# Optimization experiments

Measured on AMD Instinct MI355X. Metric: run time of the kernel, lower is better.

Reference implementation:

```python
import jax, jax.numpy as jnp
import numpy as np

B, S, H, L, NH, F, V, K, R = 64, 512, 256, 4, 8, 1024, 50265, 8, 25
DH = H // NH
EPS = 1e-5


def layernorm(x, g, b):
    mu = x.mean(-1, keepdims=True)
    var = ((x - mu) ** 2).mean(-1, keepdims=True)
    return (x - mu) * jax.lax.rsqrt(var + EPS) * g + b


def setup_inputs() -> dict:
    key = jax.random.key(0)
    ks = jax.random.split(key, 24)
    input_ids = jax.random.randint(ks[0], (B, S), 0, V, dtype=jnp.int64)
    # prefix attention mask with variable valid lengths (ragged sequences)
    lengths = jax.random.randint(ks[1], (B,), 16, S + 1)
    attention_mask = (jnp.arange(S)[None, :] < lengths[:, None]).astype(jnp.int32)
    sub_indices = jax.random.randint(ks[2], (B, K), 0, S, dtype=jnp.int64)
    obj_indices = jax.random.randint(ks[3], (B, K), 0, S, dtype=jnp.int64)
    sub_counts = jax.random.randint(ks[4], (B,), 0, K + 1, dtype=jnp.int32)
    obj_counts = jax.random.randint(ks[5], (B,), 0, K + 1, dtype=jnp.int32)
    sc = 0.02
    p = {
        'emb': jax.random.normal(ks[6], (V, H), jnp.float32) * sc,
        'Wqkv': jax.random.normal(ks[7], (L, H, 3 * H), jnp.float32) * sc,
        'bqkv': jnp.zeros((L, 3 * H), jnp.float32),
        'Wo': jax.random.normal(ks[8], (L, H, H), jnp.float32) * sc,
        'bo': jnp.zeros((L, H), jnp.float32),
        'ln1_g': jnp.ones((L, H), jnp.float32), 'ln1_b': jnp.zeros((L, H), jnp.float32),
        'ln2_g': jnp.ones((L, H), jnp.float32), 'ln2_b': jnp.zeros((L, H), jnp.float32),
        'W1': jax.random.normal(ks[9], (L, H, F), jnp.float32) * sc,
        'b1': jnp.zeros((L, F), jnp.float32),
        'W2': jax.random.normal(ks[10], (L, F, H), jnp.float32) * sc,
        'b2': jnp.zeros((L, H), jnp.float32),
        'lnf_g': jnp.ones((H,), jnp.float32), 'lnf_b': jnp.zeros((H,), jnp.float32),
        'mW1': jax.random.normal(ks[11], (3 * H, H), jnp.float32) * sc,
        'mb1': jnp.zeros((H,), jnp.float32),
        'mW2': jax.random.normal(ks[12], (H, R), jnp.float32) * sc,
        'mb2': jnp.zeros((R,), jnp.float32),
    }
    return dict(input_ids=input_ids, attention_mask=attention_mask,
                sub_indices=sub_indices, sub_counts=sub_counts,
                obj_indices=obj_indices, obj_counts=obj_counts, **p)


def _encoder(input_ids, attention_mask, emb, Wqkv, bqkv, Wo, bo,
             ln1_g, ln1_b, ln2_g, ln2_b, W1, b1, W2, b2, lnf_g, lnf_b):
    x = emb[input_ids]  # [B,S,H]
    kbias = jnp.where(attention_mask[:, None, None, :] > 0, 0.0, -1e9)  # mask keys
    scale = 1.0 / np.sqrt(DH)
    for l in range(L):  # small fixed layer loop
        qkv = x @ Wqkv[l] + bqkv[l]
        q, k, v = jnp.split(qkv, 3, axis=-1)
        q = q.reshape(B, S, NH, DH).transpose(0, 2, 1, 3)
        k = k.reshape(B, S, NH, DH).transpose(0, 2, 1, 3)
        v = v.reshape(B, S, NH, DH).transpose(0, 2, 1, 3)
        scores = jnp.einsum('bhqd,bhkd->bhqk', q, k) * scale + kbias
        attn = jax.nn.softmax(scores, axis=-1)
        o = jnp.einsum('bhqk,bhkd->bhqd', attn, v).transpose(0, 2, 1, 3).reshape(B, S, H)
        x = layernorm(x + o @ Wo[l] + bo[l], ln1_g[l], ln1_b[l])
        h = jax.nn.relu(x @ W1[l] + b1[l]) @ W2[l] + b2[l]
        x = layernorm(x + h, ln2_g[l], ln2_b[l])
    return layernorm(x, lnf_g, lnf_b)


def _pooled(seq, idx, counts):
    g = jnp.take_along_axis(seq, idx[:, :, None], axis=1)  # [B,K,H]
    m = (jnp.arange(K)[None, :] < counts[:, None]).astype(seq.dtype)
    s = (g * m[:, :, None]).sum(1)
    c = counts.astype(seq.dtype)[:, None]
    return jnp.where(c > 0, s / jnp.maximum(c, 1.0), 0.0)  # zeros if no indices


def reference(input_ids, attention_mask, sub_indices, sub_counts, obj_indices, obj_counts,
              emb, Wqkv, bqkv, Wo, bo, ln1_g, ln1_b, ln2_g, ln2_b,
              W1, b1, W2, b2, lnf_g, lnf_b, mW1, mb1, mW2, mb2):
    seq = _encoder(input_ids, attention_mask, emb, Wqkv, bqkv, Wo, bo,
                   ln1_g, ln1_b, ln2_g, ln2_b, W1, b1, W2, b2, lnf_g, lnf_b)
    sub = _pooled(seq, sub_indices, sub_counts)
    obj = _pooled(seq, obj_indices, obj_counts)
    mask = attention_mask.astype(seq.dtype)
    lens = mask.sum(1)[:, None]
    story = jnp.where(lens > 0, (seq * mask[:, :, None]).sum(1) / jnp.maximum(lens, 1.0),
                      seq.mean(1))
    feat = jnp.concatenate([sub, obj, story], axis=-1)  # [B,3H]
    logits = jax.nn.relu(feat @ mW1 + mb1) @ mW2 + mb2
    return logits
```

## Files before the change

kernel.cpp:

```cpp
#include <hip/hip_runtime.h>
#include <hip/hip_bf16.h>


typedef __hip_bfloat16 bf16;
typedef __attribute__((ext_vector_type(8))) short short8;
typedef __attribute__((ext_vector_type(4))) float f32x4;

#define S_LEN 512
#define H_DIM 256
#define NTOK  32768
#define QSCALE 0.25503488f

__device__ __forceinline__ void gload_lds16(const void* g, void* l) {
  __builtin_amdgcn_global_load_lds(
      (const __attribute__((address_space(1))) unsigned int*)g,
      (__attribute__((address_space(3))) unsigned int*)l, 16, 0, 0);
}

__device__ __forceinline__ unsigned short f2bu(float x) {
  bf16 t = __float2bfloat16(x);
  return *reinterpret_cast<unsigned short*>(&t);
}

__global__ __launch_bounds__(64) void lens_kernel(
    const int* __restrict__ amask, int* __restrict__ ntiles,
    int* __restrict__ lenb) {
  const int b = blockIdx.x, t = threadIdx.x;
  int c = 0;
#pragma unroll
  for (int i = 0; i < 8; ++i) c += amask[b * S_LEN + t + i * 64];
#pragma unroll
  for (int off = 1; off < 64; off <<= 1) c += __shfl_xor(c, off);
  if (t == 0) {
    lenb[b] = c;
    ntiles[b] = (c + 63) >> 6;
  }
}

__global__ __launch_bounds__(64) void order_kernel(
    const int* __restrict__ ntiles, int* __restrict__ ordb) {
  const int b = threadIdx.x;
  const int ntb = ntiles[b];
  int rank = 0;
  for (int j = 0; j < 64; ++j) {
    const int ntj = __shfl(ntb, j);
    rank += (ntj > ntb) || (ntj == ntb && j < b);
  }
  ordb[rank] = b;
}

__global__ __launch_bounds__(256) void tcast_kernel(
    const float* __restrict__ in, bf16* __restrict__ out, int K, int N) {
  const int l = blockIdx.z;
  in  += (size_t)l * K * N;
  out += (size_t)l * K * N;
  __shared__ float t[32][33];
  const int n0 = blockIdx.x * 32, k0 = blockIdx.y * 32;
  const int c = threadIdx.x & 31, r = threadIdx.x >> 5;
#pragma unroll
  for (int rr = r; rr < 32; rr += 8)
    t[rr][c] = in[(size_t)(k0 + rr) * N + n0 + c];
  __syncthreads();
#pragma unroll
  for (int rr = r; rr < 32; rr += 8)
    out[(size_t)(n0 + rr) * K + k0 + c] = __float2bfloat16(t[c][rr]);
}

__global__ __launch_bounds__(256) void embed_kernel(
    const int* __restrict__ ids, const float* __restrict__ emb,
    float* __restrict__ X, bf16* __restrict__ Xb) {
  size_t i4 = (size_t)blockIdx.x * 256 + threadIdx.x;
  int tok = (int)(i4 >> 6);
  int d4  = (int)(i4 & 63);
  float4 v = *(const float4*)&emb[(size_t)ids[tok] * H_DIM + d4 * 4];
  *(float4*)&X[i4 * 4] = v;
  ushort4 pk;
  pk.x = f2bu(v.x); pk.y = f2bu(v.y); pk.z = f2bu(v.z); pk.w = f2bu(v.w);
  *(ushort4*)&Xb[i4 * 4] = pk;
}

#define SRC_CHUNK(tid_) (((tid_) & 3) ^ (((tid_) >> 3) & 3))

template<int MODE, bool RELU>
__global__ __launch_bounds__(256) void hgemm_kernel(
    const bf16* __restrict__ A, const bf16* __restrict__ Bt,
    const float* __restrict__ bias, float* __restrict__ Cf,
    bf16* __restrict__ Cb, bf16* __restrict__ Vt,
    int M, int N, int K) {
  __shared__ __align__(16) bf16 As[2][4096];
  __shared__ __align__(16) bf16 Bs[2][4096];
  const int tid = threadIdx.x;
  const int wv = tid >> 6, ln = tid & 63;
  const int fr = ln & 15, g4 = ln >> 4;
  const int wr = wv >> 1, wc = wv & 1;
  const int m0 = blockIdx.x * 128, n0 = blockIdx.y * 128;
  const int lr = tid >> 2;
  const int lk = SRC_CHUNK(tid) * 8;
  const int rc = (g4 ^ ((fr >> 1) & 3)) * 8;

#define STAGE_G(buf, kk) do {                                                  \
    const int kof_ = (kk) * 32;                                                \
    gload_lds16(A  + (size_t)(m0 + lr) * K + kof_ + lk,                        \
                &As[(buf)][wv * 512]);                                         \
    gload_lds16(A  + (size_t)(m0 + 64 + lr) * K + kof_ + lk,                   \
                &As[(buf)][2048 + wv * 512]);                                  \
    gload_lds16(Bt + (size_t)(n0 + lr) * K + kof_ + lk,                        \
                &Bs[(buf)][wv * 512]);                                         \
    gload_lds16(Bt + (size_t)(n0 + 64 + lr) * K + kof_ + lk,                   \
                &Bs[(buf)][2048 + wv * 512]);                                  \
  } while (0)

  f32x4 acc[4][4];
#pragma unroll
  for (int i = 0; i < 4; ++i)
#pragma unroll
    for (int j = 0; j < 4; ++j)
      acc[i][j] = (f32x4){0.f, 0.f, 0.f, 0.f};

  const int NT = K >> 5;
  STAGE_G(0, 0);
  __syncthreads();
  int cur = 0;
  for (int kt = 0; kt < NT; ++kt) {
    if (kt + 1 < NT) STAGE_G(cur ^ 1, kt + 1);
    short8 af[4], bfv[4];
#pragma unroll
    for (int i = 0; i < 4; ++i)
      af[i] = *(const short8*)&As[cur][(wr * 64 + i * 16 + fr) * 32 + rc];
#pragma unroll
    for (int j = 0; j < 4; ++j)
      bfv[j] = *(const short8*)&Bs[cur][(wc * 64 + j * 16 + fr) * 32 + rc];
#pragma unroll
    for (int i = 0; i < 4; ++i)
#pragma unroll
      for (int j = 0; j < 4; ++j)
        acc[i][j] = __builtin_amdgcn_mfma_f32_16x16x32_bf16(
            af[i], bfv[j], acc[i][j], 0, 0, 0);
    __syncthreads();
    cur ^= 1;
  }
#undef STAGE_G

  const int crow = g4 * 4, ccol = fr;
#pragma unroll
  for (int j = 0; j < 4; ++j) {
    const int n = n0 + wc * 64 + j * 16 + ccol;
    const float bv = bias[n];
#pragma unroll
    for (int i = 0; i < 4; ++i) {
      const int mbase = m0 + wr * 64 + i * 16 + crow;
#pragma unroll
      for (int r = 0; r < 4; ++r) {
        float o = acc[i][j][r] + bv;
        if (RELU) o = fmaxf(o, 0.f);
        const int m = mbase + r;
        if (MODE == 1) {
          Cb[(size_t)m * N + n] = __float2bfloat16(o);
        } else {
          if (n < 512) {
            const float oo = (n < 256) ? o * QSCALE : o;
            Cb[(size_t)m * 768 + n] = __float2bfloat16(oo);
          } else {
            const int hd = n - 512, hh = hd >> 5, dd = hd & 31;
            const int bb = m >> 9, ss = m & 511;
            const int ssw = (ss & ~63) | ((ss & 63) ^ ((dd & 7) << 3));
            Vt[(((size_t)bb * 8 + hh) * 32 + dd) * 512 + ssw] =
                __float2bfloat16(o);
          }
        }
      }
    }
  }
}

__global__ __launch_bounds__(256) void hgemm_ln_kernel(
    const bf16* __restrict__ A, const bf16* __restrict__ Bt,
    const float* __restrict__ bias, float* __restrict__ X,
    bf16* __restrict__ Xb, const float* __restrict__ g,
    const float* __restrict__ bt, int K) {
  __shared__ __align__(16) bf16 As[2][2048];
  __shared__ __align__(16) bf16 Bs[2][8192];
  __shared__ float rsum[4][64];
  __shared__ float rsq[4][64];
  const int tid = threadIdx.x;
  const int wv = tid >> 6;
  const int ln = tid & 63;
  const int fr = ln & 15, g4 = ln >> 4;
  const int m0 = blockIdx.x * 64;
  const int rc = (g4 ^ ((fr >> 1) & 3)) * 8;

#define STAGE_L(buf, kk) do {                                                  \
    const int kof_ = (kk) * 32;                                                \
    gload_lds16(A + (size_t)(m0 + (tid >> 2)) * K + kof_ +                     \
                    SRC_CHUNK(tid) * 8,                                        \
                &As[(buf)][wv * 512]);                                         \
    _Pragma("unroll")                                                          \
    for (int e = 0; e < 4; ++e) {                                              \
      const int vt = e * 256 + tid;                                            \
      gload_lds16(Bt + (size_t)(vt >> 2) * K + kof_ + SRC_CHUNK(vt) * 8,       \
                  &Bs[(buf)][e * 2048 + wv * 512]);                            \
    }                                                                          \
  } while (0)

  f32x4 acc[4][4];
#pragma unroll
  for (int i = 0; i < 4; ++i)
#pragma unroll
    for (int j = 0; j < 4; ++j)
      acc[i][j] = (f32x4){0.f, 0.f, 0.f, 0.f};

  const int NT = K >> 5;
  STAGE_L(0, 0);
  __syncthreads();
  int cur = 0;
  for (int kt = 0; kt < NT; ++kt) {
    if (kt + 1 < NT) STAGE_L(cur ^ 1, kt + 1);
    short8 af[4], bfv[4];
#pragma unroll
    for (int i = 0; i < 4; ++i)
      af[i] = *(const short8*)&As[cur][(i * 16 + fr) * 32 + rc];
#pragma unroll
    for (int j = 0; j < 4; ++j)
      bfv[j] = *(const short8*)&Bs[cur][(wv * 64 + j * 16 + fr) * 32 + rc];
#pragma unroll
    for (int i = 0; i < 4; ++i)
#pragma unroll
      for (int j = 0; j < 4; ++j)
        acc[i][j] = __builtin_amdgcn_mfma_f32_16x16x32_bf16(
            af[i], bfv[j], acc[i][j], 0, 0, 0);
    __syncthreads();
    cur ^= 1;
  }
#undef STAGE_L

  float gj[4], bj[4], bsj[4];
#pragma unroll
  for (int j = 0; j < 4; ++j) {
    const int n = wv * 64 + j * 16 + fr;
    gj[j] = g[n]; bj[j] = bt[n]; bsj[j] = bias[n];
  }
#pragma unroll
  for (int i = 0; i < 4; ++i) {
#pragma unroll
    for (int r = 0; r < 4; ++r) {
      const int m = m0 + i * 16 + g4 * 4 + r;
#pragma unroll
      for (int j = 0; j < 4; ++j)
        acc[i][j][r] += bsj[j] + X[(size_t)m * 256 + wv * 64 + j * 16 + fr];
    }
  }
#pragma unroll
  for (int i = 0; i < 4; ++i) {
#pragma unroll
    for (int r = 0; r < 4; ++r) {
      float sp = acc[i][0][r] + acc[i][1][r] + acc[i][2][r] + acc[i][3][r];
      float qp = acc[i][0][r] * acc[i][0][r] + acc[i][1][r] * acc[i][1][r] +
                 acc[i][2][r] * acc[i][2][r] + acc[i][3][r] * acc[i][3][r];
#pragma unroll
      for (int off = 1; off < 16; off <<= 1) {
        sp += __shfl_xor(sp, off);
        qp += __shfl_xor(qp, off);
      }
      if (fr == 0) {
        const int ri = i * 16 + g4 * 4 + r;
        rsum[wv][ri] = sp;
        rsq[wv][ri] = qp;
      }
    }
  }
  __syncthreads();
#pragma unroll
  for (int i = 0; i < 4; ++i) {
#pragma unroll
    for (int r = 0; r < 4; ++r) {
      const int ri = i * 16 + g4 * 4 + r;
      const float tot = rsum[0][ri] + rsum[1][ri] + rsum[2][ri] + rsum[3][ri];
      const float tq = rsq[0][ri] + rsq[1][ri] + rsq[2][ri] + rsq[3][ri];
      const float mu = tot * (1.0f / 256.0f);
      const float var = tq * (1.0f / 256.0f) - mu * mu;
      const float rstd = rsqrtf(var + 1e-5f);
      const int m = m0 + ri;
#pragma unroll
      for (int j = 0; j < 4; ++j) {
        const float o = (acc[i][j][r] - mu) * rstd * gj[j] + bj[j];
        const size_t idx = (size_t)m * 256 + wv * 64 + j * 16 + fr;
        X[idx] = o;
        Xb[idx] = __float2bfloat16(o);
      }
    }
  }
}

__global__ __launch_bounds__(256) void attn_mfma_kernel(
    const bf16* __restrict__ QKVb, const bf16* __restrict__ Vt,
    const int* __restrict__ amask, const int* __restrict__ ntiles,
    const int* __restrict__ ordb, bf16* __restrict__ Ob) {
  const int b = ordb[blockIdx.z];
  const int h = blockIdx.y, q0 = blockIdx.x * 64;
  const int tid = threadIdx.x;
  const int wv = tid >> 6, ln = tid & 63;
  const int fr = ln & 15, g4 = ln >> 4;
  const int f8 = (fr & 7) << 3;
  const int rc = (g4 ^ ((fr >> 1) & 3)) * 8;
  const int bh32 = (b * 8 + h) * 32;
  __shared__ __align__(16) bf16 Ks[2][2048];
  __shared__ __align__(16) bf16 Vs[2][2048];
  __shared__ __align__(16) bf16 Ps[4096];
  __shared__ __align__(16) float Ms[64];

  const int nt = ntiles[b];

#define STAGE_A(buf, kt_) do {                                                 \
    const int k0_ = (kt_) * 64;                                                \
    gload_lds16(QKVb + (size_t)(b * S_LEN + k0_ + (tid >> 2)) * 768 + 256 +    \
                    h * 32 + SRC_CHUNK(tid) * 8,                               \
                &Ks[(buf)][wv * 512]);                                         \
    gload_lds16(Vt + (size_t)(bh32 + (tid >> 3)) * 512 + k0_ + (tid & 7) * 8,  \
                &Vs[(buf)][wv * 512]);                                         \
    if ((kt_) == nt - 1 && tid < 64)                                           \
      Ms[tid] = (amask[b * S_LEN + k0_ + tid] != 0) ? 0.f : -1e9f;             \
  } while (0)

  gload_lds16(QKVb + (size_t)(b * S_LEN + q0 + (tid >> 2)) * 768 + h * 32 +
                  SRC_CHUNK(tid) * 8,
              &Ps[wv * 512]);
  STAGE_A(0, 0);
  __syncthreads();
  const short8 qb = *(const short8*)&Ps[(wv * 16 + fr) * 32 + rc];
  __syncthreads();

  f32x4 accO[2];
  accO[0] = (f32x4){0.f, 0.f, 0.f, 0.f};
  accO[1] = (f32x4){0.f, 0.f, 0.f, 0.f};
  float mrun = -1e30f, lrun = 0.f;
  const int srcq = 20 * g4;

  int cur = 0;
  for (int kt = 0; kt < nt; ++kt) {
    if (kt + 1 < nt) STAGE_A(cur ^ 1, kt + 1);
    const bool bnd = (kt == nt - 1);

    f32x4 st[4];
#pragma unroll
    for (int kb = 0; kb < 4; ++kb) {
      const short8 kf = *(const short8*)&Ks[cur][(kb * 16 + fr) * 32 + rc];
      f32x4 z = (f32x4){0.f, 0.f, 0.f, 0.f};
      st[kb] = __builtin_amdgcn_mfma_f32_16x16x32_bf16(kf, qb, z, 0, 0, 0);
    }

    float p[16];
    if (bnd) {
#pragma unroll
      for (int kb = 0; kb < 4; ++kb) {
        const f32x4 mv = ((const f32x4*)Ms)[kb * 4 + g4];
#pragma unroll
        for (int rr = 0; rr < 4; ++rr) p[kb * 4 + rr] = st[kb][rr] + mv[rr];
      }
    } else {
#pragma unroll
      for (int kb = 0; kb < 4; ++kb)
#pragma unroll
        for (int rr = 0; rr < 4; ++rr) p[kb * 4 + rr] = st[kb][rr];
    }

    const float a0 = fmaxf(fmaxf(p[0], p[1]), p[2]);
    const float a1 = fmaxf(fmaxf(p[3], p[4]), p[5]);
    const float a2 = fmaxf(fmaxf(p[6], p[7]), p[8]);
    const float a3 = fmaxf(fmaxf(p[9], p[10]), p[11]);
    const float a4 = fmaxf(fmaxf(p[12], p[13]), p[14]);
    float mx = fmaxf(fmaxf(fmaxf(a0, a1), fmaxf(a2, a3)), fmaxf(a4, p[15]));
    mx = fmaxf(mx, __shfl_xor(mx, 16));
    mx = fmaxf(mx, __shfl_xor(mx, 32));

    float corr = 1.f;
    if (!__all(mx <= mrun + 8.f)) {
      const float mnew = fmaxf(mrun, mx);
      corr = exp2f(mrun - mnew);
      mrun = mnew;
#pragma unroll
      for (int rr = 0; rr < 4; ++rr) {
        const float cs = __shfl(corr, srcq + rr);
        accO[0][rr] *= cs;
        accO[1][rr] *= cs;
      }
    }

#pragma unroll
    for (int i = 0; i < 16; ++i) p[i] = exp2f(p[i] - mrun);
    const float b0 = p[0] + p[1], b1 = p[2] + p[3], b2 = p[4] + p[5],
                b3 = p[6] + p[7], b4 = p[8] + p[9], b5 = p[10] + p[11],
                b6 = p[12] + p[13], b7 = p[14] + p[15];
    float ps = ((b0 + b1) + (b2 + b3)) + ((b4 + b5) + (b6 + b7));
    ps += __shfl_xor(ps, 16);
    ps += __shfl_xor(ps, 32);
    lrun = lrun * corr + ps;

#pragma unroll
    for (int kb = 0; kb < 4; ++kb) {
      ushort4 w4;
      w4.x = f2bu(p[kb * 4 + 0]);
      w4.y = f2bu(p[kb * 4 + 1]);
      w4.z = f2bu(p[kb * 4 + 2]);
      w4.w = f2bu(p[kb * 4 + 3]);
      *(ushort4*)&Ps[wv * 1024 + fr * 64 + ((kb * 16 + g4 * 4) ^ f8)] = w4;
    }

#pragma unroll
    for (int kk = 0; kk < 2; ++kk) {
      const short8 pa = *(const short8*)
          &Ps[wv * 1024 + fr * 64 + ((kk * 32 + g4 * 8) ^ f8)];
#pragma unroll
      for (int df = 0; df < 2; ++df) {
        const short8 vb = *(const short8*)
            &Vs[cur][(df * 16 + fr) * 64 + ((kk * 32 + g4 * 8) ^ f8)];
        accO[df] = __builtin_amdgcn_mfma_f32_16x16x32_bf16(
            pa, vb, accO[df], 0, 0, 0);
      }
    }
    __syncthreads();
    cur ^= 1;
  }
#undef STAGE_A

  const float inv = 1.0f / lrun;
#pragma unroll
  for (int rr = 0; rr < 4; ++rr) {
    const float iv = __shfl(inv, srcq + rr);
    const int q = q0 + wv * 16 + g4 * 4 + rr;
    const size_t orow = ((size_t)b * S_LEN + q) * H_DIM + h * 32;
    Ob[orow + fr]      = __float2bfloat16(accO[0][rr] * iv);
    Ob[orow + 16 + fr] = __float2bfloat16(accO[1][rr] * iv);
  }
}

__global__ __launch_bounds__(256) void lnf_pool_kernel(
    float* __restrict__ X, const float* __restrict__ g,
    const float* __restrict__ bt, const int* __restrict__ amask,
    float* __restrict__ Pstory) {
  const int b = blockIdx.x, sg = blockIdx.y;
  const int tid = threadIdx.x, wv = tid >> 6, ln = tid & 63;
  const float4 gg = ((const float4*)g)[ln];
  const float4 bb = ((const float4*)bt)[ln];
  float ax = 0.f, ay = 0.f, az = 0.f, aw = 0.f;
  for (int t = wv; t < 64; t += 4) {
    const size_t tok = (size_t)b * S_LEN + sg * 64 + t;
    float4 v = ((const float4*)X)[tok * 64 + ln];
    float s = v.x + v.y + v.z + v.w;
#pragma unroll
    for (int off = 1; off < 64; off <<= 1) s += __shfl_xor(s, off);
    const float mu = s * (1.0f / 256.0f);
    const float dx = v.x - mu, dy = v.y - mu, dz = v.z - mu, dw = v.w - mu;
    float sq = dx * dx + dy * dy + dz * dz + dw * dw;
#pragma unroll
    for (int off = 1; off < 64; off <<= 1) sq += __shfl_xor(sq, off);
    const float rstd = rsqrtf(sq * (1.0f / 256.0f) + 1e-5f);
    float4 o;
    o.x = dx * rstd * gg.x + bb.x;
    o.y = dy * rstd * gg.y + bb.y;
    o.z = dz * rstd * gg.z + bb.z;
    o.w = dw * rstd * gg.w + bb.w;
    ((float4*)X)[tok * 64 + ln] = o;
    if (amask[tok]) { ax += o.x; ay += o.y; az += o.z; aw += o.w; }
  }
  __shared__ float part[4][256];
  part[wv][ln * 4 + 0] = ax;
  part[wv][ln * 4 + 1] = ay;
  part[wv][ln * 4 + 2] = az;
  part[wv][ln * 4 + 3] = aw;
  __syncthreads();
  const float tot = part[0][tid] + part[1][tid] + part[2][tid] + part[3][tid];
  Pstory[((size_t)b * 8 + sg) * 256 + tid] = tot;
}

__global__ __launch_bounds__(256) void poolcls_kernel(
    const float* __restrict__ X, const float* __restrict__ Pstory,
    const int* __restrict__ lenb,
    const int* __restrict__ sub_idx, const int* __restrict__ sub_cnt,
    const int* __restrict__ obj_idx, const int* __restrict__ obj_cnt,
    const float* __restrict__ mW1, const float* __restrict__ mb1,
    const float* __restrict__ mW2, const float* __restrict__ mb2,
    float* __restrict__ out) {
  const int b = blockIdx.x, t = threadIdx.x;
  __shared__ float fs[768];
  __shared__ float hid[256];
  const float* xb = X + (size_t)b * S_LEN * H_DIM;
  {
    float s = 0.f;
#pragma unroll
    for (int i = 0; i < 8; ++i) s += Pstory[((size_t)b * 8 + i) * 256 + t];
    fs[512 + t] = s / (float)lenb[b];
  }
  {
    const int cc = sub_cnt[b];
    float s2 = 0.f;
    for (int j = 0; j < cc; ++j)
      s2 += xb[(size_t)sub_idx[b * 8 + j] * H_DIM + t];
    fs[t] = (cc > 0) ? s2 / (float)cc : 0.f;
  }
  {
    const int cc = obj_cnt[b];
    float s2 = 0.f;
    for (int j = 0; j < cc; ++j)
      s2 += xb[(size_t)obj_idx[b * 8 + j] * H_DIM + t];
    fs[256 + t] = (cc > 0) ? s2 / (float)cc : 0.f;
  }
  __syncthreads();
  float acc = mb1[t];
  for (int k = 0; k < 768; ++k) acc += fs[k] * mW1[(size_t)k * 256 + t];
  hid[t] = fmaxf(acc, 0.f);
  __syncthreads();
  if (t < 25) {
    float o = mb2[t];
    for (int j = 0; j < 256; ++j) o += hid[j] * mW2[j * 25 + t];
    out[b * 25 + t] = o;
  }
}

extern "C" void kernel_launch(void* const* d_in, const int* in_sizes, int n_in,
                              void* d_out, int out_size, void* d_ws, size_t ws_size,
                              hipStream_t stream) {
  const int*   input_ids = (const int*)d_in[0];
  const int*   amask     = (const int*)d_in[1];
  const int*   sub_idx   = (const int*)d_in[2];
  const int*   sub_cnt   = (const int*)d_in[3];
  const int*   obj_idx   = (const int*)d_in[4];
  const int*   obj_cnt   = (const int*)d_in[5];
  const float* emb  = (const float*)d_in[6];
  const float* Wqkv = (const float*)d_in[7];
  const float* bqkv = (const float*)d_in[8];
  const float* Wo   = (const float*)d_in[9];
  const float* bo   = (const float*)d_in[10];
  const float* ln1g = (const float*)d_in[11];
  const float* ln1b = (const float*)d_in[12];
  const float* ln2g = (const float*)d_in[13];
  const float* ln2b = (const float*)d_in[14];
  const float* W1   = (const float*)d_in[15];
  const float* b1   = (const float*)d_in[16];
  const float* W2   = (const float*)d_in[17];
  const float* b2   = (const float*)d_in[18];
  const float* lnfg = (const float*)d_in[19];
  const float* lnfb = (const float*)d_in[20];
  const float* mW1  = (const float*)d_in[21];
  const float* mb1  = (const float*)d_in[22];
  const float* mW2  = (const float*)d_in[23];
  const float* mb2  = (const float*)d_in[24];
  float* out = (float*)d_out;

  char* w = (char*)d_ws;
  float* X    = (float*)w;                         w += (size_t)NTOK * 256 * 4;
  bf16*  Xb   = (bf16*)w;                          w += (size_t)NTOK * 256 * 2;
  bf16*  QKVb = (bf16*)w;                          w += (size_t)NTOK * 768 * 2;
  bf16*  Vtg  = (bf16*)w;                          w += (size_t)NTOK * 256 * 2;
  bf16*  Ob   = (bf16*)w;                          w += (size_t)NTOK * 256 * 2;
  bf16*  Wqkvt= (bf16*)w;                          w += (size_t)4 * 768 * 256 * 2;
  bf16*  Wot  = (bf16*)w;                          w += (size_t)4 * 256 * 256 * 2;
  bf16*  W1t  = (bf16*)w;                          w += (size_t)4 * 1024 * 256 * 2;
  bf16*  W2t  = (bf16*)w;                          w += (size_t)4 * 256 * 1024 * 2;
  float* Pstory = (float*)w;                       w += (size_t)64 * 8 * 256 * 4;
  int*   ntiles = (int*)w;                         w += 256;
  int*   lenb   = (int*)w;                         w += 256;
  int*   ordb   = (int*)w;                         w += 256;
  bf16*  Hb   = QKVb;

  lens_kernel<<<64, 64, 0, stream>>>(amask, ntiles, lenb);
  order_kernel<<<1, 64, 0, stream>>>(ntiles, ordb);
  tcast_kernel<<<dim3(24, 8, 4), 256, 0, stream>>>(Wqkv, Wqkvt, 256, 768);
  tcast_kernel<<<dim3(8, 8, 4), 256, 0, stream>>>(Wo, Wot, 256, 256);
  tcast_kernel<<<dim3(32, 8, 4), 256, 0, stream>>>(W1, W1t, 256, 1024);
  tcast_kernel<<<dim3(8, 32, 4), 256, 0, stream>>>(W2, W2t, 1024, 256);

  embed_kernel<<<8192, 256, 0, stream>>>(input_ids, emb, X, Xb);

  for (int l = 0; l < 4; ++l) {
    const bf16* Wqkvt_l = Wqkvt + (size_t)l * 768 * 256;
    const bf16* Wot_l   = Wot + (size_t)l * 256 * 256;
    const bf16* W1t_l   = W1t + (size_t)l * 1024 * 256;
    const bf16* W2t_l   = W2t + (size_t)l * 256 * 1024;

    hgemm_kernel<2, false><<<dim3(256, 6), 256, 0, stream>>>(
        Xb, Wqkvt_l, bqkv + (size_t)l * 768, nullptr, QKVb, Vtg, NTOK, 768, 256);
    attn_mfma_kernel<<<dim3(8, 8, 64), 256, 0, stream>>>(
        QKVb, Vtg, amask, ntiles, ordb, Ob);
    hgemm_ln_kernel<<<512, 256, 0, stream>>>(
        Ob, Wot_l, bo + (size_t)l * 256, X, Xb,
        ln1g + l * 256, ln1b + l * 256, 256);
    hgemm_kernel<1, true><<<dim3(256, 8), 256, 0, stream>>>(
        Xb, W1t_l, b1 + (size_t)l * 1024, nullptr, Hb, nullptr, NTOK, 1024, 256);
    hgemm_ln_kernel<<<512, 256, 0, stream>>>(
        Hb, W2t_l, b2 + (size_t)l * 256, X, Xb,
        ln2g + l * 256, ln2b + l * 256, 1024);
  }
  lnf_pool_kernel<<<dim3(64, 8), 256, 0, stream>>>(X, lnfg, lnfb, amask, Pstory);
  poolcls_kernel<<<64, 256, 0, stream>>>(X, Pstory, lenb, sub_idx, sub_cnt,
                                         obj_idx, obj_cnt, mW1, mb1, mW2, mb2,
                                         out);
}
```

Baseline: 791.1 us.

## Fuse FFN up-projection, ReLU, down-projection and LayerNorm into one kernel

Replaces the separate W1 GEMM and the W2 GEMM+LayerNorm kernels with a single kernel per 64-row tile. The kernel walks the 1024-wide hidden dimension in 256-column chunks, keeps each ReLU'd hidden chunk in LDS as bf16, and accumulates the W2 product in registers before applying residual, bias and LayerNorm. This removes the round trip of the large intermediate activation through global memory. In exchange, each block uses much more LDS and there are fewer blocks, so occupancy and latency hiding drop.

Measured after the change: 828.7 us. 1.05x slower.

```diff
diff --git a/kernel.cpp b/kernel.cpp
--- a/kernel.cpp
+++ b/kernel.cpp
@@ -283,6 +283,185 @@
 #pragma unroll
       for (int j = 0; j < 4; ++j) {
         const float o = (acc[i][j][r] - mu) * rstd * gj[j] + bj[j];
+        const size_t idx = (size_t)m * 256 + wv * 64 + j * 16 + fr;
+        X[idx] = o;
+        Xb[idx] = __float2bfloat16(o);
+      }
+    }
+  }
+}
+
+__global__ __launch_bounds__(256) void ffn_fused_kernel(
+    const bf16* __restrict__ Xbin, const bf16* __restrict__ W1t,
+    const float* __restrict__ b1, const bf16* __restrict__ W2t,
+    const float* __restrict__ b2, float* __restrict__ X,
+    bf16* __restrict__ Xb, const float* __restrict__ g,
+    const float* __restrict__ bt) {
+  __shared__ __align__(16) bf16 As[2][2048];
+  __shared__ __align__(16) bf16 Bs[2][8192];
+  __shared__ __align__(16) bf16 Hs[16384];
+  __shared__ float rsum[4][64];
+  __shared__ float rsq[4][64];
+  const int tid = threadIdx.x;
+  const int wv = tid >> 6, ln = tid & 63;
+  const int fr = ln & 15, g4 = ln >> 4;
+  const int m0 = blockIdx.x * 64;
+  const int rc = (g4 ^ ((fr >> 1) & 3)) * 8;
+
+#define STAGE_FA(buf, kk) do {                                                 \
+    const int kof_ = (kk) * 32;                                                \
+    gload_lds16(Xbin + (size_t)(m0 + (tid >> 2)) * 256 + kof_ +                \
+                    SRC_CHUNK(tid) * 8,                                        \
+                &As[(buf)][wv * 512]);                                         \
+    _Pragma("unroll")                                                          \
+    for (int e = 0; e < 4; ++e) {                                              \
+      const int vt = e * 256 + tid;                                            \
+      gload_lds16(W1t + (size_t)(f0 + (vt >> 2)) * 256 + kof_ +                \
+                      SRC_CHUNK(vt) * 8,                                       \
+                  &Bs[(buf)][e * 2048 + wv * 512]);                            \
+    }                                                                          \
+  } while (0)
+
+#define STAGE_FB(buf, kk) do {                                                 \
+    const int kof_ = f0 + (kk) * 32;                                           \
+    _Pragma("unroll")                                                          \
+    for (int e = 0; e < 4; ++e) {                                              \
+      const int vt = e * 256 + tid;                                            \
+      gload_lds16(W2t + (size_t)(vt >> 2) * 1024 + kof_ + SRC_CHUNK(vt) * 8,   \
+                  &Bs[(buf)][e * 2048 + wv * 512]);                            \
+    }                                                                          \
+  } while (0)
+
+  f32x4 accY[4][4];
+#pragma unroll
+  for (int i = 0; i < 4; ++i)
+#pragma unroll
+    for (int j = 0; j < 4; ++j)
+      accY[i][j] = (f32x4){0.f, 0.f, 0.f, 0.f};
+
+  for (int ch = 0; ch < 4; ++ch) {
+    const int f0 = ch * 256;
+    f32x4 accH[4][4];
+#pragma unroll
+    for (int i = 0; i < 4; ++i)
+#pragma unroll
+      for (int j = 0; j < 4; ++j)
+        accH[i][j] = (f32x4){0.f, 0.f, 0.f, 0.f};
+    STAGE_FA(0, 0);
+    __syncthreads();
+    int cur = 0;
+    for (int kt = 0; kt < 8; ++kt) {
+      if (kt + 1 < 8) STAGE_FA(cur ^ 1, kt + 1);
+      short8 af[4], bfv[4];
+#pragma unroll
+      for (int i = 0; i < 4; ++i)
+        af[i] = *(const short8*)&As[cur][(i * 16 + fr) * 32 + rc];
+#pragma unroll
+      for (int j = 0; j < 4; ++j)
+        bfv[j] = *(const short8*)&Bs[cur][(wv * 64 + j * 16 + fr) * 32 + rc];
+#pragma unroll
+      for (int i = 0; i < 4; ++i)
+#pragma unroll
+        for (int j = 0; j < 4; ++j)
+          accH[i][j] = __builtin_amdgcn_mfma_f32_16x16x32_bf16(
+              af[i], bfv[j], accH[i][j], 0, 0, 0);
+      __syncthreads();
+      cur ^= 1;
+    }
+    float bs1[4];
+#pragma unroll
+    for (int j = 0; j < 4; ++j) bs1[j] = b1[f0 + wv * 64 + j * 16 + fr];
+#pragma unroll
+    for (int i = 0; i < 4; ++i)
+#pragma unroll
+      for (int r = 0; r < 4; ++r) {
+        const int ml = i * 16 + g4 * 4 + r;
+#pragma unroll
+        for (int j = 0; j < 4; ++j) {
+          const int c = wv * 64 + j * 16 + fr;
+          const float h = fmaxf(accH[i][j][r] + bs1[j], 0.f);
+          const int ccp = (c >> 3) ^ (ml & 7);
+          Hs[ml * 256 + ccp * 8 + (c & 7)] = __float2bfloat16(h);
+        }
+      }
+    __syncthreads();
+    STAGE_FB(0, 0);
+    __syncthreads();
+    cur = 0;
+    for (int kt = 0; kt < 8; ++kt) {
+      if (kt + 1 < 8) STAGE_FB(cur ^ 1, kt + 1);
+      short8 af[4], bfv[4];
+#pragma unroll
+      for (int i = 0; i < 4; ++i) {
+        const int ccp = (kt * 4 + g4) ^ (fr & 7);
+        af[i] = *(const short8*)&Hs[(i * 16 + fr) * 256 + ccp * 8];
+      }
+#pragma unroll
+      for (int j = 0; j < 4; ++j)
+        bfv[j] = *(const short8*)&Bs[cur][(wv * 64 + j * 16 + fr) * 32 + rc];
+#pragma unroll
+      for (int i = 0; i < 4; ++i)
+#pragma unroll
+        for (int j = 0; j < 4; ++j)
+          accY[i][j] = __builtin_amdgcn_mfma_f32_16x16x32_bf16(
+              af[i], bfv[j], accY[i][j], 0, 0, 0);
+      __syncthreads();
+      cur ^= 1;
+    }
+  }
+#undef STAGE_FA
+#undef STAGE_FB
+
+  float gj[4], bj[4], bsj[4];
+#pragma unroll
+  for (int j = 0; j < 4; ++j) {
+    const int n = wv * 64 + j * 16 + fr;
+    gj[j] = g[n]; bj[j] = bt[n]; bsj[j] = b2[n];
+  }
+#pragma unroll
+  for (int i = 0; i < 4; ++i) {
+#pragma unroll
+    for (int r = 0; r < 4; ++r) {
+      const int m = m0 + i * 16 + g4 * 4 + r;
+#pragma unroll
+      for (int j = 0; j < 4; ++j)
+        accY[i][j][r] += bsj[j] + X[(size_t)m * 256 + wv * 64 + j * 16 + fr];
+    }
+  }
+#pragma unroll
+  for (int i = 0; i < 4; ++i) {
+#pragma unroll
+    for (int r = 0; r < 4; ++r) {
+      float sp = accY[i][0][r] + accY[i][1][r] + accY[i][2][r] + accY[i][3][r];
+      float qp = accY[i][0][r] * accY[i][0][r] + accY[i][1][r] * accY[i][1][r] +
+                 accY[i][2][r] * accY[i][2][r] + accY[i][3][r] * accY[i][3][r];
+#pragma unroll
+      for (int off = 1; off < 16; off <<= 1) {
+        sp += __shfl_xor(sp, off);
+        qp += __shfl_xor(qp, off);
+      }
+      if (fr == 0) {
+        const int ri = i * 16 + g4 * 4 + r;
+        rsum[wv][ri] = sp;
+        rsq[wv][ri] = qp;
+      }
+    }
+  }
+  __syncthreads();
+#pragma unroll
+  for (int i = 0; i < 4; ++i) {
+#pragma unroll
+    for (int r = 0; r < 4; ++r) {
+      const int ri = i * 16 + g4 * 4 + r;
+      const float tot = rsum[0][ri] + rsum[1][ri] + rsum[2][ri] + rsum[3][ri];
+      const float tq = rsq[0][ri] + rsq[1][ri] + rsq[2][ri] + rsq[3][ri];
+      const float mu = tot * (1.0f / 256.0f);
+      const float var = tq * (1.0f / 256.0f) - mu * mu;
+      const float rstd = rsqrtf(var + 1e-5f);
+      const int m = m0 + ri;
+#pragma unroll
+      for (int j = 0; j < 4; ++j) {
+        const float o = (accY[i][j][r] - mu) * rstd * gj[j] + bj[j];
         const size_t idx = (size_t)m * 256 + wv * 64 + j * 16 + fr;
         X[idx] = o;
         Xb[idx] = __float2bfloat16(o);
@@ -560,7 +739,6 @@
   int*   ntiles = (int*)w;                         w += 256;
   int*   lenb   = (int*)w;                         w += 256;
   int*   ordb   = (int*)w;                         w += 256;
-  bf16*  Hb   = QKVb;
 
   lens_kernel<<<64, 64, 0, stream>>>(amask, ntiles, lenb);
   order_kernel<<<1, 64, 0, stream>>>(ntiles, ordb);
@@ -584,11 +762,9 @@
     hgemm_ln_kernel<<<512, 256, 0, stream>>>(
         Ob, Wot_l, bo + (size_t)l * 256, X, Xb,
         ln1g + l * 256, ln1b + l * 256, 256);
-    hgemm_kernel<1, true><<<dim3(256, 8), 256, 0, stream>>>(
-        Xb, W1t_l, b1 + (size_t)l * 1024, nullptr, Hb, nullptr, NTOK, 1024, 256);
-    hgemm_ln_kernel<<<512, 256, 0, stream>>>(
-        Hb, W2t_l, b2 + (size_t)l * 256, X, Xb,
-        ln2g + l * 256, ln2b + l * 256, 1024);
+    ffn_fused_kernel<<<512, 256, 0, stream>>>(
+        Xb, W1t_l, b1 + (size_t)l * 1024, W2t_l, b2 + (size_t)l * 256,
+        X, Xb, ln2g + l * 256, ln2b + l * 256);
   }
   lnf_pool_kernel<<<dim3(64, 8), 256, 0, stream>>>(X, lnfg, lnfb, amask, Pstory);
   poolcls_kernel<<<64, 256, 0, stream>>>(X, Pstory, lenb, sub_idx, sub_cnt,
```

## Process four query tiles per attention block to reuse staged K/V tiles

Applied to the files above, without the earlier changes.

Each attention workgroup now handles 256 query rows, four 64-row sub-tiles, instead of 64. Every K/V tile staged into LDS is therefore reused for four query tiles, cutting global loads of K/V and the number of staging and barrier steps. In exchange the grid shrinks fourfold to 1024 blocks, and per-thread register use rises with four sets of accumulators, running max and running sum, which may lower occupancy. All four sub-tiles also share one key-tile count, so query sub-tiles still run the full key loop.

Measured after the change: 825.1 us. 1.04x slower.

```diff
diff --git a/kernel.cpp b/kernel.cpp
--- a/kernel.cpp
+++ b/kernel.cpp
@@ -296,7 +296,8 @@
     const int* __restrict__ amask, const int* __restrict__ ntiles,
     const int* __restrict__ ordb, bf16* __restrict__ Ob) {
   const int b = ordb[blockIdx.z];
-  const int h = blockIdx.y, q0 = blockIdx.x * 64;
+  const int h = blockIdx.y;
+  const int q_base = blockIdx.x * 256;
   const int tid = threadIdx.x;
   const int wv = tid >> 6, ln = tid & 63;
   const int fr = ln & 15, g4 = ln >> 4;
@@ -321,18 +322,31 @@
       Ms[tid] = (amask[b * S_LEN + k0_ + tid] != 0) ? 0.f : -1e9f;             \
   } while (0)
 
-  gload_lds16(QKVb + (size_t)(b * S_LEN + q0 + (tid >> 2)) * 768 + h * 32 +
-                  SRC_CHUNK(tid) * 8,
-              &Ps[wv * 512]);
   STAGE_A(0, 0);
-  __syncthreads();
-  const short8 qb = *(const short8*)&Ps[(wv * 16 + fr) * 32 + rc];
-  __syncthreads();
-
-  f32x4 accO[2];
-  accO[0] = (f32x4){0.f, 0.f, 0.f, 0.f};
-  accO[1] = (f32x4){0.f, 0.f, 0.f, 0.f};
-  float mrun = -1e30f, lrun = 0.f;
+
+  short8 qb[4];
+#pragma unroll
+  for (int t2 = 0; t2 < 2; ++t2) {
+    gload_lds16(QKVb + (size_t)(b * S_LEN + q_base + t2 * 128 + (tid >> 2)) *
+                        768 + h * 32 + SRC_CHUNK(tid) * 8,
+                &Ps[wv * 512]);
+    gload_lds16(QKVb + (size_t)(b * S_LEN + q_base + t2 * 128 + 64 +
+                                (tid >> 2)) * 768 + h * 32 + SRC_CHUNK(tid) * 8,
+                &Ps[2048 + wv * 512]);
+    __syncthreads();
+    qb[t2 * 2]     = *(const short8*)&Ps[(wv * 16 + fr) * 32 + rc];
+    qb[t2 * 2 + 1] = *(const short8*)&Ps[2048 + (wv * 16 + fr) * 32 + rc];
+    __syncthreads();
+  }
+
+  f32x4 accO[4][2];
+#pragma unroll
+  for (int t = 0; t < 4; ++t) {
+    accO[t][0] = (f32x4){0.f, 0.f, 0.f, 0.f};
+    accO[t][1] = (f32x4){0.f, 0.f, 0.f, 0.f};
+  }
+  float mrun[4] = {-1e30f, -1e30f, -1e30f, -1e30f};
+  float lrun[4] = {0.f, 0.f, 0.f, 0.f};
   const int srcq = 20 * g4;
 
   int cur = 0;
@@ -340,81 +354,85 @@
     if (kt + 1 < nt) STAGE_A(cur ^ 1, kt + 1);
     const bool bnd = (kt == nt - 1);
 
-    f32x4 st[4];
-#pragma unroll
-    for (int kb = 0; kb < 4; ++kb) {
-      const short8 kf = *(const short8*)&Ks[cur][(kb * 16 + fr) * 32 + rc];
-      f32x4 z = (f32x4){0.f, 0.f, 0.f, 0.f};
-      st[kb] = __builtin_amdgcn_mfma_f32_16x16x32_bf16(kf, qb, z, 0, 0, 0);
-    }
-
-    float p[16];
-    if (bnd) {
+#pragma unroll
+    for (int t = 0; t < 4; ++t) {
+      f32x4 st[4];
 #pragma unroll
       for (int kb = 0; kb < 4; ++kb) {
-        const f32x4 mv = ((const f32x4*)Ms)[kb * 4 + g4];
-#pragma unroll
-        for (int rr = 0; rr < 4; ++rr) p[kb * 4 + rr] = st[kb][rr] + mv[rr];
-      }
-    } else {
-#pragma unroll
-      for (int kb = 0; kb < 4; ++kb)
-#pragma unroll
-        for (int rr = 0; rr < 4; ++rr) p[kb * 4 + rr] = st[kb][rr];
-    }
-
-    const float a0 = fmaxf(fmaxf(p[0], p[1]), p[2]);
-    const float a1 = fmaxf(fmaxf(p[3], p[4]), p[5]);
-    const float a2 = fmaxf(fmaxf(p[6], p[7]), p[8]);
-    const float a3 = fmaxf(fmaxf(p[9], p[10]), p[11]);
-    const float a4 = fmaxf(fmaxf(p[12], p[13]), p[14]);
-    float mx = fmaxf(fmaxf(fmaxf(a0, a1), fmaxf(a2, a3)), fmaxf(a4, p[15]));
-    mx = fmaxf(mx, __shfl_xor(mx, 16));
-    mx = fmaxf(mx, __shfl_xor(mx, 32));
-
-    float corr = 1.f;
-    if (!__all(mx <= mrun + 8.f)) {
-      const float mnew = fmaxf(mrun, mx);
-      corr = exp2f(mrun - mnew);
-      mrun = mnew;
-#pragma unroll
-      for (int rr = 0; rr < 4; ++rr) {
-        const float cs = __shfl(corr, srcq + rr);
-        accO[0][rr] *= cs;
-        accO[1][rr] *= cs;
-      }
-    }
-
-#pragma unroll
-    for (int i = 0; i < 16; ++i) p[i] = exp2f(p[i] - mrun);
-    const float b0 = p[0] + p[1], b1 = p[2] + p[3], b2 = p[4] + p[5],
-                b3 = p[6] + p[7], b4 = p[8] + p[9], b5 = p[10] + p[11],
-                b6 = p[12] + p[13], b7 = p[14] + p[15];
-    float ps = ((b0 + b1) + (b2 + b3)) + ((b4 + b5) + (b6 + b7));
-    ps += __shfl_xor(ps, 16);
-    ps += __shfl_xor(ps, 32);
-    lrun = lrun * corr + ps;
-
-#pragma unroll
-    for (int kb = 0; kb < 4; ++kb) {
-      ushort4 w4;
-      w4.x = f2bu(p[kb * 4 + 0]);
-      w4.y = f2bu(p[kb * 4 + 1]);
-      w4.z = f2bu(p[kb * 4 + 2]);
-      w4.w = f2bu(p[kb * 4 + 3]);
-      *(ushort4*)&Ps[wv * 1024 + fr * 64 + ((kb * 16 + g4 * 4) ^ f8)] = w4;
-    }
-
-#pragma unroll
-    for (int kk = 0; kk < 2; ++kk) {
-      const short8 pa = *(const short8*)
-          &Ps[wv * 1024 + fr * 64 + ((kk * 32 + g4 * 8) ^ f8)];
-#pragma unroll
-      for (int df = 0; df < 2; ++df) {
-        const short8 vb = *(const short8*)
-            &Vs[cur][(df * 16 + fr) * 64 + ((kk * 32 + g4 * 8) ^ f8)];
-        accO[df] = __builtin_amdgcn_mfma_f32_16x16x32_bf16(
-            pa, vb, accO[df], 0, 0, 0);
+        const short8 kf =
+            *(const short8*)&Ks[cur][(kb * 16 + fr) * 32 + rc];
+        f32x4 z = (f32x4){0.f, 0.f, 0.f, 0.f};
+        st[kb] = __builtin_amdgcn_mfma_f32_16x16x32_bf16(kf, qb[t], z, 0, 0, 0);
+      }
+
+      float p[16];
+      if (bnd) {
+#pragma unroll
+        for (int kb = 0; kb < 4; ++kb) {
+          const f32x4 mv = ((const f32x4*)Ms)[kb * 4 + g4];
+#pragma unroll
+          for (int rr = 0; rr < 4; ++rr) p[kb * 4 + rr] = st[kb][rr] + mv[rr];
+        }
+      } else {
+#pragma unroll
+        for (int kb = 0; kb < 4; ++kb)
+#pragma unroll
+          for (int rr = 0; rr < 4; ++rr) p[kb * 4 + rr] = st[kb][rr];
+      }
+
+      const float a0 = fmaxf(fmaxf(p[0], p[1]), p[2]);
+      const float a1 = fmaxf(fmaxf(p[3], p[4]), p[5]);
+      const float a2 = fmaxf(fmaxf(p[6], p[7]), p[8]);
+      const float a3 = fmaxf(fmaxf(p[9], p[10]), p[11]);
+      const float a4 = fmaxf(fmaxf(p[12], p[13]), p[14]);
+      float mx = fmaxf(fmaxf(fmaxf(a0, a1), fmaxf(a2, a3)), fmaxf(a4, p[15]));
+      mx = fmaxf(mx, __shfl_xor(mx, 16));
+      mx = fmaxf(mx, __shfl_xor(mx, 32));
+
+      float corr = 1.f;
+      if (!__all(mx <= mrun[t] + 8.f)) {
+        const float mnew = fmaxf(mrun[t], mx);
+        corr = exp2f(mrun[t] - mnew);
+        mrun[t] = mnew;
+#pragma unroll
+        for (int rr = 0; rr < 4; ++rr) {
+          const float cs = __shfl(corr, srcq + rr);
+          accO[t][0][rr] *= cs;
+          accO[t][1][rr] *= cs;
+        }
+      }
+
+#pragma unroll
+      for (int i = 0; i < 16; ++i) p[i] = exp2f(p[i] - mrun[t]);
+      const float b0 = p[0] + p[1], b1 = p[2] + p[3], b2 = p[4] + p[5],
+                  b3 = p[6] + p[7], b4 = p[8] + p[9], b5 = p[10] + p[11],
+                  b6 = p[12] + p[13], b7 = p[14] + p[15];
+      float ps = ((b0 + b1) + (b2 + b3)) + ((b4 + b5) + (b6 + b7));
+      ps += __shfl_xor(ps, 16);
+      ps += __shfl_xor(ps, 32);
+      lrun[t] = lrun[t] * corr + ps;
+
+#pragma unroll
+      for (int kb = 0; kb < 4; ++kb) {
+        ushort4 w4;
+        w4.x = f2bu(p[kb * 4 + 0]);
+        w4.y = f2bu(p[kb * 4 + 1]);
+        w4.z = f2bu(p[kb * 4 + 2]);
+        w4.w = f2bu(p[kb * 4 + 3]);
+        *(ushort4*)&Ps[wv * 1024 + fr * 64 + ((kb * 16 + g4 * 4) ^ f8)] = w4;
+      }
+
+#pragma unroll
+      for (int kk = 0; kk < 2; ++kk) {
+        const short8 pa = *(const short8*)
+            &Ps[wv * 1024 + fr * 64 + ((kk * 32 + g4 * 8) ^ f8)];
+#pragma unroll
+        for (int df = 0; df < 2; ++df) {
+          const short8 vb = *(const short8*)
+              &Vs[cur][(df * 16 + fr) * 64 + ((kk * 32 + g4 * 8) ^ f8)];
+          accO[t][df] = __builtin_amdgcn_mfma_f32_16x16x32_bf16(
+              pa, vb, accO[t][df], 0, 0, 0);
+        }
       }
     }
     __syncthreads();
@@ -422,14 +440,17 @@
   }
 #undef STAGE_A
 
-  const float inv = 1.0f / lrun;
-#pragma unroll
-  for (int rr = 0; rr < 4; ++rr) {
-    const float iv = __shfl(inv, srcq + rr);
-    const int q = q0 + wv * 16 + g4 * 4 + rr;
-    const size_t orow = ((size_t)b * S_LEN + q) * H_DIM + h * 32;
-    Ob[orow + fr]      = __float2bfloat16(accO[0][rr] * iv);
-    Ob[orow + 16 + fr] = __float2bfloat16(accO[1][rr] * iv);
+#pragma unroll
+  for (int t = 0; t < 4; ++t) {
+    const float inv = 1.0f / lrun[t];
+#pragma unroll
+    for (int rr = 0; rr < 4; ++rr) {
+      const float iv = __shfl(inv, srcq + rr);
+      const int q = q_base + t * 64 + wv * 16 + g4 * 4 + rr;
+      const size_t orow = ((size_t)b * S_LEN + q) * H_DIM + h * 32;
+      Ob[orow + fr]      = __float2bfloat16(accO[t][0][rr] * iv);
+      Ob[orow + 16 + fr] = __float2bfloat16(accO[t][1][rr] * iv);
+    }
   }
 }
 
@@ -579,7 +600,7 @@
 
     hgemm_kernel<2, false><<<dim3(256, 6), 256, 0, stream>>>(
         Xb, Wqkvt_l, bqkv + (size_t)l * 768, nullptr, QKVb, Vtg, NTOK, 768, 256);
-    attn_mfma_kernel<<<dim3(8, 8, 64), 256, 0, stream>>>(
+    attn_mfma_kernel<<<dim3(2, 8, 64), 256, 0, stream>>>(
         QKVb, Vtg, amask, ntiles, ordb, Ob);
     hgemm_ln_kernel<<<512, 256, 0, stream>>>(
         Ob, Wot_l, bo + (size_t)l * 256, X, Xb,
```
